# Kernel tuning notes

Measured on AMD Instinct MI355X. Metric: run time of the kernel, lower is better.

Reference implementation:

```python
import jax, jax.numpy as jnp
import numpy as np

N_EMBED = 1024
HEAD_SIZE = 64
BLOCK_SIZE = 2048


def setup_inputs() -> dict:
    key = jax.random.key(0)
    kx, kk, kv = jax.random.split(key, 3)
    x = jax.random.normal(kx, (8, 2048, N_EMBED), dtype=jnp.float32)
    # nn.Linear(n_embed, head_size, bias=False): weight [head_size, n_embed]
    scale = 1.0 / np.sqrt(N_EMBED)
    W_k = jax.random.uniform(kk, (HEAD_SIZE, N_EMBED), dtype=jnp.float32, minval=-scale, maxval=scale)
    W_v = jax.random.uniform(kv, (HEAD_SIZE, N_EMBED), dtype=jnp.float32, minval=-scale, maxval=scale)
    return {"x": x, "W_k": W_k, "W_v": W_v}


def reference(x, W_k, W_v):
    # Faithful to source: q = self.key(x) (query projection is unused in the original forward)
    T = x.shape[1]
    k = jnp.einsum('btc,hc->bth', x, W_k)   # [B,T,H]
    q = k                                    # source bug: q uses key projection
    wei = jnp.einsum('bth,bsh->bts', q, k) * (HEAD_SIZE ** -0.5)  # [B,T,T]
    causal = jnp.tril(jnp.ones((T, T), dtype=bool))
    wei = jnp.where(causal, wei, -jnp.inf)
    wei = jax.nn.softmax(wei, axis=-1)
    v = jnp.einsum('btc,hc->bth', x, W_v)
    out = jnp.einsum('bts,bsh->bth', wei, v)
    return out
```

## Files before the change

### kernel.cpp

```cpp
#include <hip/hip_runtime.h>


typedef __bf16 bf16;
typedef __bf16 bf16x8 __attribute__((ext_vector_type(8)));
typedef float  floatx4 __attribute__((ext_vector_type(4)));

#define T_LEN 2048
#define HEAD  64
#define CEMB  1024

static __device__ __forceinline__ bf16x8 cvt2(float4 a, float4 b) {
    bf16x8 r;
    r[0] = (bf16)a.x; r[1] = (bf16)a.y; r[2] = (bf16)a.z; r[3] = (bf16)a.w;
    r[4] = (bf16)b.x; r[5] = (bf16)b.y; r[6] = (bf16)b.z; r[7] = (bf16)b.w;
    return r;
}

__global__ __launch_bounds__(256) void proj_kernel(const float* __restrict__ x,
                                                   const float* __restrict__ Wk,
                                                   const float* __restrict__ Wv,
                                                   bf16* __restrict__ Kbuf,
                                                   bf16* __restrict__ Vt) {
    __shared__ __align__(16) bf16 As[32][72];
    __shared__ __align__(16) bf16 Bs[64][72];

    const int tid  = threadIdx.x;
    const int wave = tid >> 6;
    const int lane = tid & 63;
    const int quad = lane >> 4;
    const int low  = lane & 15;

    const int mblk  = blockIdx.x >> 1;
    const int nhalf = blockIdx.x & 1;
    const long row0 = (long)mblk * 32;

    const int a_row = tid >> 3;
    const int a_col = (tid & 7) * 8;
    const int b_row = tid >> 2;
    const int b_col = (tid & 3) * 16;

    const float* abase = x + (row0 + a_row) * CEMB + a_col;
    const float* wrow  = (nhalf ? Wv : Wk) + b_row * CEMB + b_col;

    const int strip = wave & 1;
    const int npair = wave >> 1;

    floatx4 acc[2];
    acc[0] = (floatx4){0.f, 0.f, 0.f, 0.f};
    acc[1] = (floatx4){0.f, 0.f, 0.f, 0.f};

    float4 apf[2], bpf[4];
#pragma unroll
    for (int i = 0; i < 2; ++i) apf[i] = ((const float4*)abase)[i];
#pragma unroll
    for (int i = 0; i < 4; ++i) bpf[i] = ((const float4*)wrow)[i];

    for (int s = 0; s < 16; ++s) {
        __syncthreads();
        *(bf16x8*)&As[a_row][a_col] = cvt2(apf[0], apf[1]);
        *(bf16x8*)&Bs[b_row][b_col]     = cvt2(bpf[0], bpf[1]);
        *(bf16x8*)&Bs[b_row][b_col + 8] = cvt2(bpf[2], bpf[3]);
        if (s < 15) {
            const int k0 = (s + 1) * 64;
#pragma unroll
            for (int i = 0; i < 2; ++i) apf[i] = ((const float4*)(abase + k0))[i];
#pragma unroll
            for (int i = 0; i < 4; ++i) bpf[i] = ((const float4*)(wrow + k0))[i];
        }
        __syncthreads();

#pragma unroll
        for (int h = 0; h < 2; ++h) {
            bf16x8 afrag = *(const bf16x8*)&As[strip * 16 + low][h * 32 + quad * 8];
#pragma unroll
            for (int i = 0; i < 2; ++i) {
                bf16x8 bfrag = *(const bf16x8*)&Bs[(npair * 2 + i) * 16 + low][h * 32 + quad * 8];
                acc[i] = __builtin_amdgcn_mfma_f32_16x16x32_bf16(afrag, bfrag, acc[i], 0, 0, 0);
            }
        }
    }

#pragma unroll
    for (int i = 0; i < 2; ++i) {
#pragma unroll
        for (int r = 0; r < 4; ++r) {
            long trow = row0 + strip * 16 + quad * 4 + r;
            long b    = trow >> 11;
            int  tloc = (int)(trow & 2047);
            int  cl   = (npair * 2 + i) * 16 + low;
            bf16 val  = (bf16)acc[i][r];
            if (nhalf == 0) Kbuf[(b * T_LEN + tloc) * HEAD + cl] = val;
            else            Vt[(b * HEAD + cl) * T_LEN + tloc]   = val;
        }
    }
}

__global__ __launch_bounds__(256) void attn_kernel(const bf16* __restrict__ Kbuf,
                                                   const bf16* __restrict__ Vt,
                                                   float* __restrict__ Opart,
                                                   float* __restrict__ lpart) {
    __shared__ __align__(16) bf16 Qs[64][72];
    __shared__ __align__(16) bf16 Ks[64][72];
    __shared__ __align__(16) bf16 Vs[64][72];
    __shared__ __align__(16) bf16 Ps[64][72];

    const int tid  = threadIdx.x;
    const int wave = tid >> 6;
    const int lane = tid & 63;
    const int quad = lane >> 4;
    const int low  = lane & 15;

    const int c  = blockIdx.x & 3;
    const int qb = (blockIdx.x >> 2) & 31;
    const int b  = blockIdx.x >> 7;

    const bf16* kbase = Kbuf + (long)b * T_LEN * HEAD;
    const bf16* vbase = Vt + (long)b * HEAD * T_LEN;

    const int s_row = tid >> 2;
    const int s_col = (tid & 3) * 16;

    {
        const bf16* src = kbase + (qb * 64 + s_row) * HEAD + s_col;
        *(float4*)&Qs[s_row][s_col]     = *(const float4*)(src);
        *(float4*)&Qs[s_row][s_col + 8] = *(const float4*)(src + 8);
    }
    __syncthreads();
    const bf16x8 qf0 = *(const bf16x8*)&Qs[wave * 16 + low][quad * 8];
    const bf16x8 qf1 = *(const bf16x8*)&Qs[wave * 16 + low][32 + quad * 8];

    bf16x8 ones;
#pragma unroll
    for (int i = 0; i < 8; ++i) ones[i] = (bf16)1.0f;

    floatx4 o[4], ol;
#pragma unroll
    for (int nt = 0; nt < 4; ++nt) o[nt] = (floatx4){0.f, 0.f, 0.f, 0.f};
    ol = (floatx4){0.f, 0.f, 0.f, 0.f};

    const bf16* ksrc = kbase + s_row * HEAD + s_col;
    const bf16* vsrc = vbase + (long)s_row * T_LEN + s_col;

    if (c <= qb) {
        float4 kpf0 = *(const float4*)(ksrc + c * 4096);
        float4 kpf1 = *(const float4*)(ksrc + c * 4096 + 8);
        float4 vpf0 = *(const float4*)(vsrc + c * 64);
        float4 vpf1 = *(const float4*)(vsrc + c * 64 + 8);

        for (int j = c; j <= qb; j += 4) {
            __syncthreads();
            *(float4*)&Ks[s_row][s_col]     = kpf0;
            *(float4*)&Ks[s_row][s_col + 8] = kpf1;
            *(float4*)&Vs[s_row][s_col]     = vpf0;
            *(float4*)&Vs[s_row][s_col + 8] = vpf1;
            if (j + 4 <= qb) {
                kpf0 = *(const float4*)(ksrc + (j + 4) * 4096);
                kpf1 = *(const float4*)(ksrc + (j + 4) * 4096 + 8);
                vpf0 = *(const float4*)(vsrc + (j + 4) * 64);
                vpf1 = *(const float4*)(vsrc + (j + 4) * 64 + 8);
            }
            __syncthreads();

            floatx4 s_[4];
#pragma unroll
            for (int nt = 0; nt < 4; ++nt) {
                bf16x8 kf0 = *(const bf16x8*)&Ks[nt * 16 + low][quad * 8];
                bf16x8 kf1 = *(const bf16x8*)&Ks[nt * 16 + low][32 + quad * 8];
                floatx4 z = (floatx4){0.f, 0.f, 0.f, 0.f};
                z = __builtin_amdgcn_mfma_f32_16x16x32_bf16(qf0, kf0, z, 0, 0, 0);
                z = __builtin_amdgcn_mfma_f32_16x16x32_bf16(qf1, kf1, z, 0, 0, 0);
                s_[nt] = z;
            }

            const bool diag = (j == qb);
#pragma unroll
            for (int nt = 0; nt < 4; ++nt) {
#pragma unroll
                for (int r = 0; r < 4; ++r) {
                    float p = __builtin_amdgcn_exp2f(s_[nt][r] * 0.180336880f);
                    if (diag && (nt * 16 + low) > (wave * 16 + quad * 4 + r)) p = 0.f;
                    Ps[wave * 16 + quad * 4 + r][nt * 16 + low] = (bf16)p;
                }
            }

            bf16x8 pf0 = *(const bf16x8*)&Ps[wave * 16 + low][quad * 8];
            bf16x8 pf1 = *(const bf16x8*)&Ps[wave * 16 + low][32 + quad * 8];
#pragma unroll
            for (int nt = 0; nt < 4; ++nt) {
                bf16x8 vf0 = *(const bf16x8*)&Vs[nt * 16 + low][quad * 8];
                bf16x8 vf1 = *(const bf16x8*)&Vs[nt * 16 + low][32 + quad * 8];
                o[nt] = __builtin_amdgcn_mfma_f32_16x16x32_bf16(pf0, vf0, o[nt], 0, 0, 0);
                o[nt] = __builtin_amdgcn_mfma_f32_16x16x32_bf16(pf1, vf1, o[nt], 0, 0, 0);
            }
            ol = __builtin_amdgcn_mfma_f32_16x16x32_bf16(pf0, ones, ol, 0, 0, 0);
            ol = __builtin_amdgcn_mfma_f32_16x16x32_bf16(pf1, ones, ol, 0, 0, 0);
        }
    }

    float* ob = Opart + (long)blockIdx.x * 4096;
#pragma unroll
    for (int nt = 0; nt < 4; ++nt) {
#pragma unroll
        for (int r = 0; r < 4; ++r) {
            int row = wave * 16 + quad * 4 + r;
            ob[row * 64 + nt * 16 + low] = o[nt][r];
        }
    }
    if (low == 0) {
#pragma unroll
        for (int r = 0; r < 4; ++r)
            lpart[(long)blockIdx.x * 64 + wave * 16 + quad * 4 + r] = ol[r];
    }
}

__global__ __launch_bounds__(256) void attn_combine(const float* __restrict__ Opart,
                                                    const float* __restrict__ lpart,
                                                    float* __restrict__ out) {
    const int tile = blockIdx.x;
    const int tid  = threadIdx.x;
    const int row  = tid >> 2;
    const int col0 = (tid & 3) * 16;

    const float* ob = Opart + (long)tile * 4 * 4096 + row * 64 + col0;
    const float* lb = lpart + (long)tile * 4 * 64 + row;

    float l = lb[0] + lb[64] + lb[128] + lb[192];
    float rl = 1.0f / l;

    float4 s0 = (float4){0.f, 0.f, 0.f, 0.f}, s1 = s0, s2 = s0, s3 = s0;
#pragma unroll
    for (int ch = 0; ch < 4; ++ch) {
        const float4* p = (const float4*)(ob + ch * 4096);
        float4 a = p[0], b = p[1], c = p[2], d = p[3];
        s0.x += a.x; s0.y += a.y; s0.z += a.z; s0.w += a.w;
        s1.x += b.x; s1.y += b.y; s1.z += b.z; s1.w += b.w;
        s2.x += c.x; s2.y += c.y; s2.z += c.z; s2.w += c.w;
        s3.x += d.x; s3.y += d.y; s3.z += d.z; s3.w += d.w;
    }
    s0.x *= rl; s0.y *= rl; s0.z *= rl; s0.w *= rl;
    s1.x *= rl; s1.y *= rl; s1.z *= rl; s1.w *= rl;
    s2.x *= rl; s2.y *= rl; s2.z *= rl; s2.w *= rl;
    s3.x *= rl; s3.y *= rl; s3.z *= rl; s3.w *= rl;

    float4* op = (float4*)(out + (long)tile * 4096 + row * 64 + col0);
    op[0] = s0; op[1] = s1; op[2] = s2; op[3] = s3;
}

extern "C" void kernel_launch(void* const* d_in, const int* in_sizes, int n_in,
                              void* d_out, int out_size, void* d_ws, size_t ws_size,
                              hipStream_t stream) {
    const float* x  = (const float*)d_in[0];
    const float* Wk = (const float*)d_in[1];
    const float* Wv = (const float*)d_in[2];
    float* out = (float*)d_out;

    char* ws = (char*)d_ws;
    bf16*  Kbuf  = (bf16*)ws;
    bf16*  Vt    = (bf16*)(ws + (2 << 20));
    float* Opart = (float*)(ws + (4 << 20));
    float* lpart = (float*)(ws + (20 << 20));

    proj_kernel<<<1024, 256, 0, stream>>>(x, Wk, Wv, Kbuf, Vt);
    attn_kernel<<<1024, 256, 0, stream>>>(Kbuf, Vt, Opart, lpart);
    attn_combine<<<256, 256, 0, stream>>>(Opart, lpart, out);
}
```

Baseline: 149.1 us.

## Pre-convert weights, fuse K/V projection, double-buffer tiles, split attention eight ways

A new small kernel converts Wk and Wv to bf16 once per call. The projection kernel then computes K and V in the same block, so each x tile is read and converted only once, and it double-buffers shared memory to drop one barrier per step. The attention kernel loads Q fragments straight from global memory, double-buffers the K and V tiles, and splits the key range eight ways instead of four, giving twice as many blocks. The combine kernel sums eight partials in exchange, which means more partial-output traffic, plus one extra kernel launch.

```diff
diff --git a/kernel.cpp b/kernel.cpp
--- a/kernel.cpp
+++ b/kernel.cpp
@@ -2,6 +2,7 @@
 
 
 typedef __bf16 bf16;
+typedef __bf16 bf16x4 __attribute__((ext_vector_type(4)));
 typedef __bf16 bf16x8 __attribute__((ext_vector_type(8)));
 typedef float  floatx4 __attribute__((ext_vector_type(4)));
 
@@ -16,13 +17,23 @@
     return r;
 }
 
+__global__ __launch_bounds__(256) void wconv_kernel(const float* __restrict__ Wk,
+                                                    const float* __restrict__ Wv,
+                                                    bf16* __restrict__ Wb) {
+    int i = (blockIdx.x * 256 + threadIdx.x) * 4;
+    const float* src = (i < 64 * 1024) ? (Wk + i) : (Wv + (i - 64 * 1024));
+    float4 f = *(const float4*)src;
+    bf16x4 v;
+    v[0] = (bf16)f.x; v[1] = (bf16)f.y; v[2] = (bf16)f.z; v[3] = (bf16)f.w;
+    *(bf16x4*)&Wb[i] = v;
+}
+
 __global__ __launch_bounds__(256) void proj_kernel(const float* __restrict__ x,
-                                                   const float* __restrict__ Wk,
-                                                   const float* __restrict__ Wv,
+                                                   const bf16* __restrict__ Wb,
                                                    bf16* __restrict__ Kbuf,
                                                    bf16* __restrict__ Vt) {
-    __shared__ __align__(16) bf16 As[32][72];
-    __shared__ __align__(16) bf16 Bs[64][72];
+    __shared__ __align__(16) bf16 As[2][32][72];
+    __shared__ __align__(16) bf16 Bs[2][128][72];
 
     const int tid  = threadIdx.x;
     const int wave = tid >> 6;
@@ -30,67 +41,74 @@
     const int quad = lane >> 4;
     const int low  = lane & 15;
 
-    const int mblk  = blockIdx.x >> 1;
-    const int nhalf = blockIdx.x & 1;
-    const long row0 = (long)mblk * 32;
+    const long row0 = (long)blockIdx.x * 32;
 
     const int a_row = tid >> 3;
     const int a_col = (tid & 7) * 8;
-    const int b_row = tid >> 2;
-    const int b_col = (tid & 3) * 16;
+    const int b_row = tid >> 1;
+    const int b_col = (tid & 1) * 32;
 
     const float* abase = x + (row0 + a_row) * CEMB + a_col;
-    const float* wrow  = (nhalf ? Wv : Wk) + b_row * CEMB + b_col;
+    const bf16*  bbase = Wb + b_row * CEMB + b_col;
 
     const int strip = wave & 1;
-    const int npair = wave >> 1;
-
-    floatx4 acc[2];
-    acc[0] = (floatx4){0.f, 0.f, 0.f, 0.f};
-    acc[1] = (floatx4){0.f, 0.f, 0.f, 0.f};
-
-    float4 apf[2], bpf[4];
-#pragma unroll
-    for (int i = 0; i < 2; ++i) apf[i] = ((const float4*)abase)[i];
-#pragma unroll
-    for (int i = 0; i < 4; ++i) bpf[i] = ((const float4*)wrow)[i];
-
+    const int nq    = (wave >> 1) * 4;
+
+    floatx4 acc[4];
+#pragma unroll
+    for (int i = 0; i < 4; ++i) acc[i] = (floatx4){0.f, 0.f, 0.f, 0.f};
+
+    float4 apf0 = ((const float4*)abase)[0], apf1 = ((const float4*)abase)[1];
+    float4 bpf0 = ((const float4*)bbase)[0], bpf1 = ((const float4*)bbase)[1];
+    float4 bpf2 = ((const float4*)bbase)[2], bpf3 = ((const float4*)bbase)[3];
+    *(bf16x8*)&As[0][a_row][a_col] = cvt2(apf0, apf1);
+    *(float4*)&Bs[0][b_row][b_col]      = bpf0;
+    *(float4*)&Bs[0][b_row][b_col + 8]  = bpf1;
+    *(float4*)&Bs[0][b_row][b_col + 16] = bpf2;
+    *(float4*)&Bs[0][b_row][b_col + 24] = bpf3;
+    __syncthreads();
+
+    int buf = 0;
     for (int s = 0; s < 16; ++s) {
-        __syncthreads();
-        *(bf16x8*)&As[a_row][a_col] = cvt2(apf[0], apf[1]);
-        *(bf16x8*)&Bs[b_row][b_col]     = cvt2(bpf[0], bpf[1]);
-        *(bf16x8*)&Bs[b_row][b_col + 8] = cvt2(bpf[2], bpf[3]);
-        if (s < 15) {
+        const bool more = (s < 15);
+        if (more) {
             const int k0 = (s + 1) * 64;
-#pragma unroll
-            for (int i = 0; i < 2; ++i) apf[i] = ((const float4*)(abase + k0))[i];
-#pragma unroll
-            for (int i = 0; i < 4; ++i) bpf[i] = ((const float4*)(wrow + k0))[i];
-        }
-        __syncthreads();
-
-#pragma unroll
-        for (int h = 0; h < 2; ++h) {
-            bf16x8 afrag = *(const bf16x8*)&As[strip * 16 + low][h * 32 + quad * 8];
-#pragma unroll
-            for (int i = 0; i < 2; ++i) {
-                bf16x8 bfrag = *(const bf16x8*)&Bs[(npair * 2 + i) * 16 + low][h * 32 + quad * 8];
+            apf0 = ((const float4*)(abase + k0))[0]; apf1 = ((const float4*)(abase + k0))[1];
+            bpf0 = ((const float4*)(bbase + k0))[0]; bpf1 = ((const float4*)(bbase + k0))[1];
+            bpf2 = ((const float4*)(bbase + k0))[2]; bpf3 = ((const float4*)(bbase + k0))[3];
+        }
+#pragma unroll
+        for (int ks = 0; ks < 2; ++ks) {
+            bf16x8 afrag = *(const bf16x8*)&As[buf][strip * 16 + low][ks * 32 + quad * 8];
+#pragma unroll
+            for (int i = 0; i < 4; ++i) {
+                bf16x8 bfrag = *(const bf16x8*)&Bs[buf][(nq + i) * 16 + low][ks * 32 + quad * 8];
                 acc[i] = __builtin_amdgcn_mfma_f32_16x16x32_bf16(afrag, bfrag, acc[i], 0, 0, 0);
             }
         }
-    }
-
-#pragma unroll
-    for (int i = 0; i < 2; ++i) {
+        if (more) {
+            const int nb = buf ^ 1;
+            *(bf16x8*)&As[nb][a_row][a_col] = cvt2(apf0, apf1);
+            *(float4*)&Bs[nb][b_row][b_col]      = bpf0;
+            *(float4*)&Bs[nb][b_row][b_col + 8]  = bpf1;
+            *(float4*)&Bs[nb][b_row][b_col + 16] = bpf2;
+            *(float4*)&Bs[nb][b_row][b_col + 24] = bpf3;
+            __syncthreads();
+            buf = nb;
+        }
+    }
+
+    const long bidx  = row0 >> 11;
+    const int  tloc0 = (int)(row0 & 2047);
+#pragma unroll
+    for (int i = 0; i < 4; ++i) {
 #pragma unroll
         for (int r = 0; r < 4; ++r) {
-            long trow = row0 + strip * 16 + quad * 4 + r;
-            long b    = trow >> 11;
-            int  tloc = (int)(trow & 2047);
-            int  cl   = (npair * 2 + i) * 16 + low;
-            bf16 val  = (bf16)acc[i][r];
-            if (nhalf == 0) Kbuf[(b * T_LEN + tloc) * HEAD + cl] = val;
-            else            Vt[(b * HEAD + cl) * T_LEN + tloc]   = val;
+            int trow = tloc0 + strip * 16 + quad * 4 + r;
+            int cl   = (nq + i) * 16 + low;
+            bf16 val = (bf16)acc[i][r];
+            if (cl < HEAD) Kbuf[(bidx * T_LEN + trow) * HEAD + cl] = val;
+            else           Vt[(bidx * HEAD + (cl - HEAD)) * T_LEN + trow] = val;
         }
     }
 }
@@ -99,9 +117,8 @@
                                                    const bf16* __restrict__ Vt,
                                                    float* __restrict__ Opart,
                                                    float* __restrict__ lpart) {
-    __shared__ __align__(16) bf16 Qs[64][72];
-    __shared__ __align__(16) bf16 Ks[64][72];
-    __shared__ __align__(16) bf16 Vs[64][72];
+    __shared__ __align__(16) bf16 Ks[2][64][72];
+    __shared__ __align__(16) bf16 Vs[2][64][72];
     __shared__ __align__(16) bf16 Ps[64][72];
 
     const int tid  = threadIdx.x;
@@ -110,34 +127,28 @@
     const int quad = lane >> 4;
     const int low  = lane & 15;
 
-    const int c  = blockIdx.x & 3;
-    const int qb = (blockIdx.x >> 2) & 31;
-    const int b  = blockIdx.x >> 7;
+    const int c  = blockIdx.x & 7;
+    const int qb = (blockIdx.x >> 3) & 31;
+    const int b  = blockIdx.x >> 8;
 
     const bf16* kbase = Kbuf + (long)b * T_LEN * HEAD;
     const bf16* vbase = Vt + (long)b * HEAD * T_LEN;
 
+    const bf16* qrow = kbase + (qb * 64 + wave * 16 + low) * HEAD + quad * 8;
+    const bf16x8 qf0 = *(const bf16x8*)(qrow);
+    const bf16x8 qf1 = *(const bf16x8*)(qrow + 32);
+
+    bf16x8 ones;
+#pragma unroll
+    for (int i = 0; i < 8; ++i) ones[i] = (bf16)1.0f;
+
+    floatx4 o[4], ol;
+#pragma unroll
+    for (int nt = 0; nt < 4; ++nt) o[nt] = (floatx4){0.f, 0.f, 0.f, 0.f};
+    ol = (floatx4){0.f, 0.f, 0.f, 0.f};
+
     const int s_row = tid >> 2;
     const int s_col = (tid & 3) * 16;
-
-    {
-        const bf16* src = kbase + (qb * 64 + s_row) * HEAD + s_col;
-        *(float4*)&Qs[s_row][s_col]     = *(const float4*)(src);
-        *(float4*)&Qs[s_row][s_col + 8] = *(const float4*)(src + 8);
-    }
-    __syncthreads();
-    const bf16x8 qf0 = *(const bf16x8*)&Qs[wave * 16 + low][quad * 8];
-    const bf16x8 qf1 = *(const bf16x8*)&Qs[wave * 16 + low][32 + quad * 8];
-
-    bf16x8 ones;
-#pragma unroll
-    for (int i = 0; i < 8; ++i) ones[i] = (bf16)1.0f;
-
-    floatx4 o[4], ol;
-#pragma unroll
-    for (int nt = 0; nt < 4; ++nt) o[nt] = (floatx4){0.f, 0.f, 0.f, 0.f};
-    ol = (floatx4){0.f, 0.f, 0.f, 0.f};
-
     const bf16* ksrc = kbase + s_row * HEAD + s_col;
     const bf16* vsrc = vbase + (long)s_row * T_LEN + s_col;
 
@@ -146,26 +157,27 @@
         float4 kpf1 = *(const float4*)(ksrc + c * 4096 + 8);
         float4 vpf0 = *(const float4*)(vsrc + c * 64);
         float4 vpf1 = *(const float4*)(vsrc + c * 64 + 8);
-
-        for (int j = c; j <= qb; j += 4) {
-            __syncthreads();
-            *(float4*)&Ks[s_row][s_col]     = kpf0;
-            *(float4*)&Ks[s_row][s_col + 8] = kpf1;
-            *(float4*)&Vs[s_row][s_col]     = vpf0;
-            *(float4*)&Vs[s_row][s_col + 8] = vpf1;
-            if (j + 4 <= qb) {
-                kpf0 = *(const float4*)(ksrc + (j + 4) * 4096);
-                kpf1 = *(const float4*)(ksrc + (j + 4) * 4096 + 8);
-                vpf0 = *(const float4*)(vsrc + (j + 4) * 64);
-                vpf1 = *(const float4*)(vsrc + (j + 4) * 64 + 8);
-            }
-            __syncthreads();
+        *(float4*)&Ks[0][s_row][s_col]     = kpf0;
+        *(float4*)&Ks[0][s_row][s_col + 8] = kpf1;
+        *(float4*)&Vs[0][s_row][s_col]     = vpf0;
+        *(float4*)&Vs[0][s_row][s_col + 8] = vpf1;
+        __syncthreads();
+
+        int buf = 0;
+        for (int j = c; j <= qb; j += 8) {
+            const bool more = (j + 8 <= qb);
+            if (more) {
+                kpf0 = *(const float4*)(ksrc + (j + 8) * 4096);
+                kpf1 = *(const float4*)(ksrc + (j + 8) * 4096 + 8);
+                vpf0 = *(const float4*)(vsrc + (j + 8) * 64);
+                vpf1 = *(const float4*)(vsrc + (j + 8) * 64 + 8);
+            }
 
             floatx4 s_[4];
 #pragma unroll
             for (int nt = 0; nt < 4; ++nt) {
-                bf16x8 kf0 = *(const bf16x8*)&Ks[nt * 16 + low][quad * 8];
-                bf16x8 kf1 = *(const bf16x8*)&Ks[nt * 16 + low][32 + quad * 8];
+                bf16x8 kf0 = *(const bf16x8*)&Ks[buf][nt * 16 + low][quad * 8];
+                bf16x8 kf1 = *(const bf16x8*)&Ks[buf][nt * 16 + low][32 + quad * 8];
                 floatx4 z = (floatx4){0.f, 0.f, 0.f, 0.f};
                 z = __builtin_amdgcn_mfma_f32_16x16x32_bf16(qf0, kf0, z, 0, 0, 0);
                 z = __builtin_amdgcn_mfma_f32_16x16x32_bf16(qf1, kf1, z, 0, 0, 0);
@@ -187,13 +199,23 @@
             bf16x8 pf1 = *(const bf16x8*)&Ps[wave * 16 + low][32 + quad * 8];
 #pragma unroll
             for (int nt = 0; nt < 4; ++nt) {
-                bf16x8 vf0 = *(const bf16x8*)&Vs[nt * 16 + low][quad * 8];
-                bf16x8 vf1 = *(const bf16x8*)&Vs[nt * 16 + low][32 + quad * 8];
+                bf16x8 vf0 = *(const bf16x8*)&Vs[buf][nt * 16 + low][quad * 8];
+                bf16x8 vf1 = *(const bf16x8*)&Vs[buf][nt * 16 + low][32 + quad * 8];
                 o[nt] = __builtin_amdgcn_mfma_f32_16x16x32_bf16(pf0, vf0, o[nt], 0, 0, 0);
                 o[nt] = __builtin_amdgcn_mfma_f32_16x16x32_bf16(pf1, vf1, o[nt], 0, 0, 0);
             }
             ol = __builtin_amdgcn_mfma_f32_16x16x32_bf16(pf0, ones, ol, 0, 0, 0);
             ol = __builtin_amdgcn_mfma_f32_16x16x32_bf16(pf1, ones, ol, 0, 0, 0);
+
+            if (more) {
+                const int nb = buf ^ 1;
+                *(float4*)&Ks[nb][s_row][s_col]     = kpf0;
+                *(float4*)&Ks[nb][s_row][s_col + 8] = kpf1;
+                *(float4*)&Vs[nb][s_row][s_col]     = vpf0;
+                *(float4*)&Vs[nb][s_row][s_col + 8] = vpf1;
+                __syncthreads();
+                buf = nb;
+            }
         }
     }
 
@@ -221,15 +243,17 @@
     const int row  = tid >> 2;
     const int col0 = (tid & 3) * 16;
 
-    const float* ob = Opart + (long)tile * 4 * 4096 + row * 64 + col0;
-    const float* lb = lpart + (long)tile * 4 * 64 + row;
-
-    float l = lb[0] + lb[64] + lb[128] + lb[192];
+    const float* ob = Opart + (long)tile * 8 * 4096 + row * 64 + col0;
+    const float* lb = lpart + (long)tile * 8 * 64 + row;
+
+    float l = 0.f;
+#pragma unroll
+    for (int ch = 0; ch < 8; ++ch) l += lb[ch * 64];
     float rl = 1.0f / l;
 
     float4 s0 = (float4){0.f, 0.f, 0.f, 0.f}, s1 = s0, s2 = s0, s3 = s0;
 #pragma unroll
-    for (int ch = 0; ch < 4; ++ch) {
+    for (int ch = 0; ch < 8; ++ch) {
         const float4* p = (const float4*)(ob + ch * 4096);
         float4 a = p[0], b = p[1], c = p[2], d = p[3];
         s0.x += a.x; s0.y += a.y; s0.z += a.z; s0.w += a.w;
@@ -255,12 +279,14 @@
     float* out = (float*)d_out;
 
     char* ws = (char*)d_ws;
-    bf16*  Kbuf  = (bf16*)ws;
-    bf16*  Vt    = (bf16*)(ws + (2 << 20));
-    float* Opart = (float*)(ws + (4 << 20));
-    float* lpart = (float*)(ws + (20 << 20));
-
-    proj_kernel<<<1024, 256, 0, stream>>>(x, Wk, Wv, Kbuf, Vt);
-    attn_kernel<<<1024, 256, 0, stream>>>(Kbuf, Vt, Opart, lpart);
+    bf16*  Wb    = (bf16*)ws;
+    bf16*  Kbuf  = (bf16*)(ws + (1 << 20));
+    bf16*  Vt    = (bf16*)(ws + (3 << 20));
+    float* Opart = (float*)(ws + (5 << 20));
+    float* lpart = (float*)(ws + (37 << 20));
+
+    wconv_kernel<<<128, 256, 0, stream>>>(Wk, Wv, Wb);
+    proj_kernel<<<512, 256, 0, stream>>>(x, Wb, Kbuf, Vt);
+    attn_kernel<<<2048, 256, 0, stream>>>(Kbuf, Vt, Opart, lpart);
     attn_combine<<<256, 256, 0, stream>>>(Opart, lpart, out);
 }
```

Measured after the change: 145.2 us. 1.03x faster.
